# Kernel tuning notes

Measured on AMD Instinct MI355X. Metric: run time of the kernel, lower is better.

## Reference

```python
import jax, jax.numpy as jnp
import numpy as np

N_NODES = 50000
N_EDGES = 800000
IN_CH = 128
HID = 128
N_CLASSES = 10
NUM_GRAPHS = 64


def setup_inputs() -> dict:
    key = jax.random.key(0)
    ks = jax.random.split(key, 16)
    x = jax.random.normal(ks[0], (N_NODES, IN_CH), dtype=jnp.float32)
    edge_index = jax.random.randint(ks[1], (2, N_EDGES), 0, N_NODES, dtype=jnp.int64)
    batch = jnp.sort(jax.random.randint(ks[2], (N_NODES,), 0, NUM_GRAPHS, dtype=jnp.int64))

    def lin(k, fan_in, fan_out):
        # torch nn.Linear default init: U(-1/sqrt(fan_in), 1/sqrt(fan_in))
        kw, kb = jax.random.split(k)
        bound = 1.0 / np.sqrt(fan_in)
        W = jax.random.uniform(kw, (fan_out, fan_in), jnp.float32, -bound, bound)
        b = jax.random.uniform(kb, (fan_out,), jnp.float32, -bound, bound)
        return W, b

    W_msg1, b_msg1 = lin(ks[3], IN_CH, HID)
    W_upd1, b_upd1 = lin(ks[4], IN_CH + HID, HID)
    W_msg2, b_msg2 = lin(ks[5], HID, HID)
    W_upd2, b_upd2 = lin(ks[6], HID + HID, HID)
    W_cls, b_cls = lin(ks[7], HID, N_CLASSES)
    return {
        "x": x, "edge_index": edge_index, "batch": batch,
        "W_msg1": W_msg1, "b_msg1": b_msg1, "W_upd1": W_upd1, "b_upd1": b_upd1,
        "W_msg2": W_msg2, "b_msg2": b_msg2, "W_upd2": W_upd2, "b_upd2": b_upd2,
        "W_cls": W_cls, "b_cls": b_cls,
    }


def _mpnn_layer(x, row, col, W_msg, b_msg, W_upd, b_upd):
    # gather -> linear message
    messages = x[col] @ W_msg.T + b_msg          # [E, out]
    # scatter-add aggregate into node buckets
    aggr = jax.ops.segment_sum(messages, row, num_segments=x.shape[0])  # [N, out]
    # concat + linear + ReLU update
    h = jnp.concatenate([x, aggr], axis=1) @ W_upd.T + b_upd
    return jax.nn.relu(h)


def reference(x, edge_index, batch,
              W_msg1, b_msg1, W_upd1, b_upd1,
              W_msg2, b_msg2, W_upd2, b_upd2,
              W_cls, b_cls):
    row, col = edge_index[0], edge_index[1]
    h = _mpnn_layer(x, row, col, W_msg1, b_msg1, W_upd1, b_upd1)
    h = _mpnn_layer(h, row, col, W_msg2, b_msg2, W_upd2, b_upd2)
    # mean pool per graph
    pooled = jax.ops.segment_sum(h, batch, num_segments=NUM_GRAPHS)   # [G, HID]
    count = jnp.bincount(batch, length=NUM_GRAPHS).astype(pooled.dtype)
    pooled = pooled / count[:, None]
    return pooled @ W_cls.T + b_cls
```

## Files before the change

kernel.cpp:

```cpp
#include <hip/hip_runtime.h>
#include <hip/hip_bf16.h>

#define N_NODES 50000
#define N_EDGES 800000
#define NUM_GRAPHS 64
#define NBUCK 391

typedef __attribute__((ext_vector_type(8))) short short8;
typedef __attribute__((ext_vector_type(16))) float f32x16;

static __device__ __forceinline__ short f2bf(float f) {
    union { __hip_bfloat16 h; short s; } u;
    u.h = __float2bfloat16(f);
    return u.s;
}
static __device__ __forceinline__ unsigned short f2bfu(float f) {
    union { __hip_bfloat16 h; unsigned short s; } u;
    u.h = __float2bfloat16(f);
    return u.s;
}
static __device__ __forceinline__ float bflo(unsigned u) { return __uint_as_float(u << 16); }
static __device__ __forceinline__ float bfhi(unsigned u) { return __uint_as_float(u & 0xffff0000u); }

__global__ void cvt_kernel(const float* __restrict__ x, uint4* __restrict__ xb, int n8) {
    int i = blockIdx.x * 256 + threadIdx.x;
    if (i >= n8) return;
    const float4* p = (const float4*)(x + (size_t)i * 8);
    float4 f0 = p[0], f1 = p[1];
    uint4 r;
    r.x = ((unsigned)f2bfu(f0.y) << 16) | f2bfu(f0.x);
    r.y = ((unsigned)f2bfu(f0.w) << 16) | f2bfu(f0.z);
    r.z = ((unsigned)f2bfu(f1.y) << 16) | f2bfu(f1.x);
    r.w = ((unsigned)f2bfu(f1.w) << 16) | f2bfu(f1.z);
    xb[i] = r;
}

__global__ void fold_kernel(const float* __restrict__ Wu1, const float* __restrict__ Wm1,
                            const float* __restrict__ bm1, short* __restrict__ Wcatf1,
                            float* __restrict__ c1,
                            const float* __restrict__ Wu2, const float* __restrict__ Wm2,
                            const float* __restrict__ bm2, short* __restrict__ Wcatf2,
                            float* __restrict__ c2) {
    int layer = blockIdx.x >> 7;
    int o = blockIdx.x & 127;
    int k = threadIdx.x;
    const float* Wu = layer ? Wu2 : Wu1;
    const float* Wm = layer ? Wm2 : Wm1;
    const float* bm = layer ? bm2 : bm1;
    short* Wcatf = layer ? Wcatf2 : Wcatf1;
    float* cvec = layer ? c2 : c1;
    float val;
    if (k < 128) {
        val = Wu[o * 256 + k];
    } else {
        int kk = k - 128;
        float s = 0.f;
        for (int j = 0; j < 128; ++j) s += Wu[o * 256 + 128 + j] * Wm[j * 128 + kk];
        val = s;
    }
    Wcatf[(((k >> 3) * 128) + o) * 8 + (k & 7)] = f2bf(val);
    if (k == 0) {
        float cs = 0.f;
        for (int j = 0; j < 128; ++j) cs += Wu[o * 256 + 128 + j] * bm[j];
        cvec[o] = cs;
    }
}

__global__ void cnt_kernel(const int* __restrict__ batch, float* __restrict__ cnt, int N) {
    __shared__ float loc[NUM_GRAPHS];
    int t = threadIdx.x;
    if (t < NUM_GRAPHS) loc[t] = 0.f;
    __syncthreads();
    int n = blockIdx.x * 256 + t;
    if (n < N) atomicAdd(&loc[batch[n]], 1.0f);
    __syncthreads();
    if (t < NUM_GRAPHS && loc[t] != 0.f) atomicAdd(&cnt[t], loc[t]);
}

__global__ __launch_bounds__(1024) void binhist_kernel(const int* __restrict__ row,
                                                       int* __restrict__ bhist, int E) {
    __shared__ int lh[NBUCK];
    int t = threadIdx.x;
    for (int i = t; i < NBUCK; i += 1024) lh[i] = 0;
    __syncthreads();
    int e0 = blockIdx.x * 4096;
#pragma unroll
    for (int k = 0; k < 4; ++k) {
        int e = e0 + k * 1024 + t;
        if (e < E) atomicAdd(&lh[row[e] >> 7], 1);
    }
    __syncthreads();
    for (int i = t; i < NBUCK; i += 1024)
        if (lh[i]) atomicAdd(&bhist[i], lh[i]);
}

__global__ void bscan_kernel(const int* __restrict__ bhist, int* __restrict__ bbase,
                             int* __restrict__ bcur) {
    __shared__ int s[512];
    int t = threadIdx.x;
    int v = (t < NBUCK) ? bhist[t] : 0;
    s[t] = v;
    __syncthreads();
    for (int o = 1; o < 512; o <<= 1) {
        int a = (t >= o) ? s[t - o] : 0;
        __syncthreads();
        s[t] += a;
        __syncthreads();
    }
    if (t <= NBUCK) bbase[t] = s[t] - ((t < NBUCK) ? bhist[t] : 0);
    if (t < NBUCK) bcur[t] = s[t] - bhist[t];
}

__global__ __launch_bounds__(1024) void binA_kernel(const int* __restrict__ row,
                                                    const int* __restrict__ col,
                                                    int* __restrict__ bcur,
                                                    unsigned* __restrict__ ebin, int E) {
    __shared__ int lcur[NBUCK];
    __shared__ int lscan[NBUCK];
    __shared__ int gbase[NBUCK];
    __shared__ int sscan[512];
    __shared__ unsigned stage[4096];
    int t = threadIdx.x;
    for (int i = t; i < NBUCK; i += 1024) lcur[i] = 0;
    __syncthreads();
    int e0 = blockIdx.x * 4096;
    unsigned pv[4];
    int pb[4], pr[4];
#pragma unroll
    for (int k = 0; k < 4; ++k) {
        int e = e0 + k * 1024 + t;
        if (e < E) {
            int r = row[e], c = col[e];
            pv[k] = ((unsigned)r << 16) | (unsigned)c;
            pb[k] = r >> 7;
            pr[k] = atomicAdd(&lcur[pb[k]], 1);
        } else {
            pb[k] = -1;
        }
    }
    __syncthreads();
    if (t < 512) sscan[t] = (t < NBUCK) ? lcur[t] : 0;
    __syncthreads();
    for (int o = 1; o < 512; o <<= 1) {
        int a = 0;
        if (t < 512 && t >= o) a = sscan[t - o];
        __syncthreads();
        if (t < 512) sscan[t] += a;
        __syncthreads();
    }
    if (t < NBUCK) lscan[t] = sscan[t] - lcur[t];
    __syncthreads();
    for (int i = t; i < NBUCK; i += 1024) {
        int c = lcur[i];
        gbase[i] = c ? atomicAdd(&bcur[i], c) : 0;
    }
#pragma unroll
    for (int k = 0; k < 4; ++k)
        if (pb[k] >= 0) stage[lscan[pb[k]] + pr[k]] = pv[k];
    __syncthreads();
    int total = E - e0;
    if (total > 4096) total = 4096;
    for (int idx = t; idx < total; idx += 1024) {
        unsigned v = stage[idx];
        int b = v >> 23;
        ebin[gbase[b] + (idx - lscan[b])] = v;
    }
}

__global__ __launch_bounds__(256) void binB_kernel(const unsigned* __restrict__ ebin,
                                                   const int* __restrict__ bbase,
                                                   const int* __restrict__ bcur,
                                                   int* __restrict__ csr,
                                                   int* __restrict__ hist,
                                                   int* __restrict__ off, int N) {
    __shared__ int lcnt[128];
    __shared__ int loff[128];
    __shared__ int lcur2[128];
    __shared__ int sscan[128];
    __shared__ unsigned short stage[4096];
    int b = blockIdx.x, t = threadIdx.x;
    int base = bbase[b];
    int n = bcur[b] - base;
    if (n > 4096) n = 4096;
    if (t < 128) lcnt[t] = 0;
    __syncthreads();
    for (int idx = t; idx < n; idx += 256) {
        unsigned v = ebin[base + idx];
        atomicAdd(&lcnt[(v >> 16) & 127], 1);
    }
    __syncthreads();
    if (t < 128) sscan[t] = lcnt[t];
    __syncthreads();
    for (int o = 1; o < 128; o <<= 1) {
        int a = 0;
        if (t < 128 && t >= o) a = sscan[t - o];
        __syncthreads();
        if (t < 128) sscan[t] += a;
        __syncthreads();
    }
    if (t < 128) {
        loff[t] = sscan[t] - lcnt[t];
        lcur2[t] = sscan[t] - lcnt[t];
    }
    __syncthreads();
    for (int idx = t; idx < n; idx += 256) {
        unsigned v = ebin[base + idx];
        int lr = (v >> 16) & 127;
        int pos = atomicAdd(&lcur2[lr], 1);
        stage[pos] = (unsigned short)(v & 0xffffu);
    }
    __syncthreads();
    for (int idx = t; idx < n; idx += 256) csr[base + idx] = (int)stage[idx];
    int r0 = b * 128;
    if (t < 128 && r0 + t < N) {
        hist[r0 + t] = lcnt[t];
        off[r0 + t] = base + loff[t];
    }
}

__global__ __launch_bounds__(256) void gather_kernel(const unsigned short* __restrict__ src,
                                                     const int* __restrict__ off,
                                                     const int* __restrict__ hist,
                                                     const int* __restrict__ csr,
                                                     unsigned int* __restrict__ aggb, int N) {
    int wave = threadIdx.x >> 6, lane = threadIdx.x & 63;
    int n = blockIdx.x * 4 + wave;
    if (n >= N) return;
    int s = off[n];
    int e = s + hist[n];
    int grp = lane >> 4, sub = lane & 15;
    float a0 = 0.f, a1 = 0.f, a2 = 0.f, a3 = 0.f, a4 = 0.f, a5 = 0.f, a6 = 0.f, a7 = 0.f;
    for (int base = s; base < e; base += 64) {
        int m = e - base;
        if (m > 64) m = 64;
        int ce = (base + lane < e) ? csr[base + lane] : 0;
        int iters = (m + 3) >> 2;
#pragma unroll 4
        for (int i = 0; i < iters; ++i) {
            int idx = i * 4 + grp;
            int c = __shfl(ce, idx);
            uint4 v = *(const uint4*)(src + (size_t)c * 128 + sub * 8);
            if (idx >= m) { v.x = 0; v.y = 0; v.z = 0; v.w = 0; }
            a0 += bflo(v.x); a1 += bfhi(v.x);
            a2 += bflo(v.y); a3 += bfhi(v.y);
            a4 += bflo(v.z); a5 += bfhi(v.z);
            a6 += bflo(v.w); a7 += bfhi(v.w);
        }
    }
#pragma unroll
    for (int mk = 16; mk <= 32; mk <<= 1) {
        a0 += __shfl_xor(a0, mk); a1 += __shfl_xor(a1, mk);
        a2 += __shfl_xor(a2, mk); a3 += __shfl_xor(a3, mk);
        a4 += __shfl_xor(a4, mk); a5 += __shfl_xor(a5, mk);
        a6 += __shfl_xor(a6, mk); a7 += __shfl_xor(a7, mk);
    }
    if (grp == 0) {
        uint4 r;
        r.x = ((unsigned)f2bfu(a1) << 16) | f2bfu(a0);
        r.y = ((unsigned)f2bfu(a3) << 16) | f2bfu(a2);
        r.z = ((unsigned)f2bfu(a5) << 16) | f2bfu(a4);
        r.w = ((unsigned)f2bfu(a7) << 16) | f2bfu(a6);
        ((uint4*)aggb)[(size_t)n * 16 + sub] = r;
    }
}

template <int POOL>
__global__ __launch_bounds__(512) void update_kernel(
    const void* __restrict__ xin_, const unsigned int* __restrict__ aggb,
    const int* __restrict__ hist, const float* __restrict__ cvec,
    const float* __restrict__ bupd, const short* __restrict__ Wcatf,
    unsigned int* __restrict__ houtb, float* __restrict__ pooled,
    const int* __restrict__ batch, int N) {
    __shared__ short lds_s[32768];
    const int tid = threadIdx.x;
    const int wave = tid >> 6, lane = tid & 63;
    const int l31 = lane & 31, hi = lane >> 5;

    {
        const uint4* g = (const uint4*)Wcatf;
        uint4* l4 = (uint4*)lds_s;
#pragma unroll
        for (int j = 0; j < 8; ++j) l4[j * 512 + tid] = g[j * 512 + tid];
    }
    __syncthreads();

    const int m0 = blockIdx.x * 256 + wave * 32;
    int nr = m0 + l31;
    if (nr >= N) nr = N - 1;
    f32x16 acc[4] = {};
#pragma unroll
    for (int step = 0; step < 16; ++step) {
        short8 a;
        if (step < 8) {
            a = *(const short8*)((const short*)xin_ + (size_t)nr * 128 + step * 16 + hi * 8);
        } else {
            a = *(const short8*)((const short*)aggb + (size_t)nr * 128 + (step - 8) * 16 + hi * 8);
        }
#pragma unroll
        for (int ct = 0; ct < 4; ++ct) {
            const short8 b = *(const short8*)(lds_s + (((step * 2 + hi) * 128) + ct * 32 + l31) * 8);
            acc[ct] = __builtin_amdgcn_mfma_f32_32x32x16_bf16(a, b, acc[ct], 0, 0, 0);
        }
    }
    __syncthreads();

    float dv[16];
#pragma unroll
    for (int r = 0; r < 16; ++r) {
        int row = (r & 3) + 8 * (r >> 2) + 4 * hi;
        int node = m0 + row;
        if (node >= N) node = N - 1;
        dv[r] = (float)hist[node];
    }
    short* tp = lds_s + wave * 4096;
#pragma unroll
    for (int ct = 0; ct < 4; ++ct) {
        int o = ct * 32 + l31;
        float co = cvec[o], bo = bupd[o];
#pragma unroll
        for (int r = 0; r < 16; ++r) {
            int row = (r & 3) + 8 * (r >> 2) + 4 * hi;
            float v = fmaxf(acc[ct][r] + dv[r] * co + bo, 0.f);
            tp[row * 128 + o] = f2bf(v);
        }
    }
    __syncthreads();

    if (POOL == 0) {
        const uint4* l4 = (const uint4*)tp;
#pragma unroll
        for (int j = 0; j < 8; ++j) {
            int node = m0 + j * 4 + (lane >> 4);
            if (node < N)
                ((uint4*)houtb)[(size_t)m0 * 16 + j * 64 + lane] = l4[j * 64 + lane];
        }
    } else {
        int c = tid & 127, seg = tid >> 7;
        int base = blockIdx.x * 256 + seg * 64;
        float s = 0.f;
        int gprev = -1;
        for (int i = 0; i < 64; ++i) {
            int node = base + i;
            if (node >= N) break;
            int g = batch[node];
            if (g != gprev) {
                if (gprev >= 0) atomicAdd(&pooled[gprev * 128 + c], s);
                s = 0.f;
                gprev = g;
            }
            unsigned u = (unsigned short)lds_s[(seg * 64 + i) * 128 + c];
            s += __uint_as_float(u << 16);
        }
        if (gprev >= 0) atomicAdd(&pooled[gprev * 128 + c], s);
    }
}

__global__ void final_kernel(const float* __restrict__ pooled, const float* __restrict__ cnt,
                             const float* __restrict__ Wcls, const float* __restrict__ bcls,
                             float* __restrict__ out) {
    __shared__ float sh[128];
    int g = blockIdx.x;
    int t = threadIdx.x;
    sh[t] = pooled[g * 128 + t] / cnt[g];
    __syncthreads();
    if (t < 10) {
        float s = bcls[t];
        for (int i = 0; i < 128; ++i) s += sh[i] * Wcls[t * 128 + i];
        out[g * 10 + t] = s;
    }
}

extern "C" void kernel_launch(void* const* d_in, const int* in_sizes, int n_in,
                              void* d_out, int out_size, void* d_ws, size_t ws_size,
                              hipStream_t stream) {
    const float* x = (const float*)d_in[0];
    const int* ei = (const int*)d_in[1];
    const int* batch = (const int*)d_in[2];
    const float* Wm1 = (const float*)d_in[3];
    const float* bm1 = (const float*)d_in[4];
    const float* Wu1 = (const float*)d_in[5];
    const float* bu1 = (const float*)d_in[6];
    const float* Wm2 = (const float*)d_in[7];
    const float* bm2 = (const float*)d_in[8];
    const float* Wu2 = (const float*)d_in[9];
    const float* bu2 = (const float*)d_in[10];
    const float* Wcls = (const float*)d_in[11];
    const float* bcls = (const float*)d_in[12];
    float* out = (float*)d_out;

    const int N = N_NODES, E = N_EDGES;
    const int* row = ei;
    const int* col = ei + E;
    const int EB = (E + 4095) / 4096;
    const int UB = (N + 255) / 256;

    int* bhist = (int*)d_ws;
    float* cnt = (float*)(bhist + 512);
    float* pooled = cnt + 64;
    int* bbase = (int*)(pooled + 8192);
    int* bcur = bbase + 512;
    int* hist = bcur + 512;
    int* off = hist + 50000;
    unsigned* ebin = (unsigned*)(off + 50000);
    int* csr = (int*)(ebin + 800000);
    unsigned* aggb = (unsigned*)(csr + 800000);
    unsigned* h1b = aggb + 3200000;
    unsigned* xb = h1b + 3200000;
    float* c1 = (float*)(xb + 3200000);
    float* c2 = c1 + 128;
    short* Wcatf1 = (short*)(c2 + 128);
    short* Wcatf2 = Wcatf1 + 32768;

    hipMemsetAsync(d_ws, 0, (size_t)(512 + 64 + 8192) * 4, stream);

    cvt_kernel<<<(800000 + 255) / 256, 256, 0, stream>>>(x, (uint4*)xb, 800000);
    fold_kernel<<<256, 256, 0, stream>>>(Wu1, Wm1, bm1, Wcatf1, c1,
                                         Wu2, Wm2, bm2, Wcatf2, c2);
    cnt_kernel<<<(N + 255) / 256, 256, 0, stream>>>(batch, cnt, N);

    binhist_kernel<<<EB, 1024, 0, stream>>>(row, bhist, E);
    bscan_kernel<<<1, 512, 0, stream>>>(bhist, bbase, bcur);
    binA_kernel<<<EB, 1024, 0, stream>>>(row, col, bcur, ebin, E);
    binB_kernel<<<NBUCK, 256, 0, stream>>>(ebin, bbase, bcur, csr, hist, off, N);

    gather_kernel<<<(N + 3) / 4, 256, 0, stream>>>((const unsigned short*)xb, off, hist,
                                                   csr, aggb, N);
    update_kernel<0><<<UB, 512, 0, stream>>>(xb, aggb, hist, c1, bu1, Wcatf1,
                                             h1b, nullptr, nullptr, N);
    gather_kernel<<<(N + 3) / 4, 256, 0, stream>>>((const unsigned short*)h1b, off, hist,
                                                   csr, aggb, N);
    update_kernel<1><<<UB, 512, 0, stream>>>(h1b, aggb, hist, c2, bu2, Wcatf2,
                                             nullptr, pooled, batch, N);

    final_kernel<<<NUM_GRAPHS, 128, 0, stream>>>(pooled, cnt, Wcls, bcls, out);
}
```

Measured before the change: 152.4 us.

## Merge prep kernels, compute graph counts by binary search, simplify gather loop

Result: faster. 143.9 us (-5.6%).

```diff
diff --git a/kernel.cpp b/kernel.cpp
--- a/kernel.cpp
+++ b/kernel.cpp
@@ -22,59 +22,55 @@
 static __device__ __forceinline__ float bflo(unsigned u) { return __uint_as_float(u << 16); }
 static __device__ __forceinline__ float bfhi(unsigned u) { return __uint_as_float(u & 0xffff0000u); }
 
-__global__ void cvt_kernel(const float* __restrict__ x, uint4* __restrict__ xb, int n8) {
-    int i = blockIdx.x * 256 + threadIdx.x;
-    if (i >= n8) return;
-    const float4* p = (const float4*)(x + (size_t)i * 8);
-    float4 f0 = p[0], f1 = p[1];
-    uint4 r;
-    r.x = ((unsigned)f2bfu(f0.y) << 16) | f2bfu(f0.x);
-    r.y = ((unsigned)f2bfu(f0.w) << 16) | f2bfu(f0.z);
-    r.z = ((unsigned)f2bfu(f1.y) << 16) | f2bfu(f1.x);
-    r.w = ((unsigned)f2bfu(f1.w) << 16) | f2bfu(f1.z);
-    xb[i] = r;
-}
-
-__global__ void fold_kernel(const float* __restrict__ Wu1, const float* __restrict__ Wm1,
-                            const float* __restrict__ bm1, short* __restrict__ Wcatf1,
-                            float* __restrict__ c1,
-                            const float* __restrict__ Wu2, const float* __restrict__ Wm2,
-                            const float* __restrict__ bm2, short* __restrict__ Wcatf2,
-                            float* __restrict__ c2) {
-    int layer = blockIdx.x >> 7;
-    int o = blockIdx.x & 127;
-    int k = threadIdx.x;
-    const float* Wu = layer ? Wu2 : Wu1;
-    const float* Wm = layer ? Wm2 : Wm1;
-    const float* bm = layer ? bm2 : bm1;
-    short* Wcatf = layer ? Wcatf2 : Wcatf1;
-    float* cvec = layer ? c2 : c1;
-    float val;
-    if (k < 128) {
-        val = Wu[o * 256 + k];
+__global__ __launch_bounds__(256) void prep_kernel(
+    const float* __restrict__ x, uint4* __restrict__ xb,
+    const float* __restrict__ Wu1, const float* __restrict__ Wm1,
+    const float* __restrict__ bm1, short* __restrict__ Wcatf1, float* __restrict__ c1,
+    const float* __restrict__ Wu2, const float* __restrict__ Wm2,
+    const float* __restrict__ bm2, short* __restrict__ Wcatf2, float* __restrict__ c2,
+    int* __restrict__ zbase) {
+    int bid = blockIdx.x, t = threadIdx.x;
+    if (bid < 3125) {
+        int i = bid * 256 + t;
+        if (i < 800000) {
+            const float4* p = (const float4*)(x + (size_t)i * 8);
+            float4 f0 = p[0], f1 = p[1];
+            uint4 r;
+            r.x = ((unsigned)f2bfu(f0.y) << 16) | f2bfu(f0.x);
+            r.y = ((unsigned)f2bfu(f0.w) << 16) | f2bfu(f0.z);
+            r.z = ((unsigned)f2bfu(f1.y) << 16) | f2bfu(f1.x);
+            r.w = ((unsigned)f2bfu(f1.w) << 16) | f2bfu(f1.z);
+            xb[i] = r;
+        }
+    } else if (bid < 3381) {
+        int lb = bid - 3125;
+        int layer = lb >> 7;
+        int o = lb & 127;
+        int k = t;
+        const float* Wu = layer ? Wu2 : Wu1;
+        const float* Wm = layer ? Wm2 : Wm1;
+        const float* bm = layer ? bm2 : bm1;
+        short* Wcatf = layer ? Wcatf2 : Wcatf1;
+        float* cvec = layer ? c2 : c1;
+        float val;
+        if (k < 128) {
+            val = Wu[o * 256 + k];
+        } else {
+            int kk = k - 128;
+            float s = 0.f;
+            for (int j = 0; j < 128; ++j) s += Wu[o * 256 + 128 + j] * Wm[j * 128 + kk];
+            val = s;
+        }
+        Wcatf[(((k >> 3) * 128) + o) * 8 + (k & 7)] = f2bf(val);
+        if (k == 0) {
+            float cs = 0.f;
+            for (int j = 0; j < 128; ++j) cs += Wu[o * 256 + 128 + j] * bm[j];
+            cvec[o] = cs;
+        }
     } else {
-        int kk = k - 128;
-        float s = 0.f;
-        for (int j = 0; j < 128; ++j) s += Wu[o * 256 + 128 + j] * Wm[j * 128 + kk];
-        val = s;
-    }
-    Wcatf[(((k >> 3) * 128) + o) * 8 + (k & 7)] = f2bf(val);
-    if (k == 0) {
-        float cs = 0.f;
-        for (int j = 0; j < 128; ++j) cs += Wu[o * 256 + 128 + j] * bm[j];
-        cvec[o] = cs;
-    }
-}
-
-__global__ void cnt_kernel(const int* __restrict__ batch, float* __restrict__ cnt, int N) {
-    __shared__ float loc[NUM_GRAPHS];
-    int t = threadIdx.x;
-    if (t < NUM_GRAPHS) loc[t] = 0.f;
-    __syncthreads();
-    int n = blockIdx.x * 256 + t;
-    if (n < N) atomicAdd(&loc[batch[n]], 1.0f);
-    __syncthreads();
-    if (t < NUM_GRAPHS && loc[t] != 0.f) atomicAdd(&cnt[t], loc[t]);
+        int i = (bid - 3381) * 256 + t;
+        if (i < 512 + 8192) zbase[i] = 0;
+    }
 }
 
 __global__ __launch_bounds__(1024) void binhist_kernel(const int* __restrict__ row,
@@ -230,22 +226,14 @@
     int e = s + hist[n];
     int grp = lane >> 4, sub = lane & 15;
     float a0 = 0.f, a1 = 0.f, a2 = 0.f, a3 = 0.f, a4 = 0.f, a5 = 0.f, a6 = 0.f, a7 = 0.f;
-    for (int base = s; base < e; base += 64) {
-        int m = e - base;
-        if (m > 64) m = 64;
-        int ce = (base + lane < e) ? csr[base + lane] : 0;
-        int iters = (m + 3) >> 2;
 #pragma unroll 4
-        for (int i = 0; i < iters; ++i) {
-            int idx = i * 4 + grp;
-            int c = __shfl(ce, idx);
-            uint4 v = *(const uint4*)(src + (size_t)c * 128 + sub * 8);
-            if (idx >= m) { v.x = 0; v.y = 0; v.z = 0; v.w = 0; }
-            a0 += bflo(v.x); a1 += bfhi(v.x);
-            a2 += bflo(v.y); a3 += bfhi(v.y);
-            a4 += bflo(v.z); a5 += bfhi(v.z);
-            a6 += bflo(v.w); a7 += bfhi(v.w);
-        }
+    for (int i = s + grp; i < e; i += 4) {
+        int c = csr[i];
+        uint4 v = *(const uint4*)(src + (size_t)c * 128 + sub * 8);
+        a0 += bflo(v.x); a1 += bfhi(v.x);
+        a2 += bflo(v.y); a3 += bfhi(v.y);
+        a4 += bflo(v.z); a5 += bfhi(v.z);
+        a6 += bflo(v.w); a7 += bfhi(v.w);
     }
 #pragma unroll
     for (int mk = 16; mk <= 32; mk <<= 1) {
@@ -355,13 +343,24 @@
     }
 }
 
-__global__ void final_kernel(const float* __restrict__ pooled, const float* __restrict__ cnt,
+__global__ void final_kernel(const float* __restrict__ pooled, const int* __restrict__ batch,
                              const float* __restrict__ Wcls, const float* __restrict__ bcls,
-                             float* __restrict__ out) {
+                             float* __restrict__ out, int N) {
     __shared__ float sh[128];
+    __shared__ int cntsh;
     int g = blockIdx.x;
     int t = threadIdx.x;
-    sh[t] = pooled[g * 128 + t] / cnt[g];
+    if (t == 0) {
+        int lo = 0, hi = N;
+        while (lo < hi) { int mid = (lo + hi) >> 1; if (batch[mid] < g) lo = mid + 1; else hi = mid; }
+        int start = lo;
+        lo = 0; hi = N;
+        while (lo < hi) { int mid = (lo + hi) >> 1; if (batch[mid] < g + 1) lo = mid + 1; else hi = mid; }
+        cntsh = lo - start;
+    }
+    __syncthreads();
+    float c = (cntsh > 0) ? (float)cntsh : 1.f;
+    sh[t] = pooled[g * 128 + t] / c;
     __syncthreads();
     if (t < 10) {
         float s = bcls[t];
@@ -395,8 +394,7 @@
     const int UB = (N + 255) / 256;
 
     int* bhist = (int*)d_ws;
-    float* cnt = (float*)(bhist + 512);
-    float* pooled = cnt + 64;
+    float* pooled = (float*)(bhist + 512);
     int* bbase = (int*)(pooled + 8192);
     int* bcur = bbase + 512;
     int* hist = bcur + 512;
@@ -411,13 +409,8 @@
     short* Wcatf1 = (short*)(c2 + 128);
     short* Wcatf2 = Wcatf1 + 32768;
 
-    hipMemsetAsync(d_ws, 0, (size_t)(512 + 64 + 8192) * 4, stream);
-
-    cvt_kernel<<<(800000 + 255) / 256, 256, 0, stream>>>(x, (uint4*)xb, 800000);
-    fold_kernel<<<256, 256, 0, stream>>>(Wu1, Wm1, bm1, Wcatf1, c1,
-                                         Wu2, Wm2, bm2, Wcatf2, c2);
-    cnt_kernel<<<(N + 255) / 256, 256, 0, stream>>>(batch, cnt, N);
-
+    prep_kernel<<<3415, 256, 0, stream>>>(x, (uint4*)xb, Wu1, Wm1, bm1, Wcatf1, c1,
+                                          Wu2, Wm2, bm2, Wcatf2, c2, bhist);
     binhist_kernel<<<EB, 1024, 0, stream>>>(row, bhist, E);
     bscan_kernel<<<1, 512, 0, stream>>>(bhist, bbase, bcur);
     binA_kernel<<<EB, 1024, 0, stream>>>(row, col, bcur, ebin, E);
@@ -432,5 +425,5 @@
     update_kernel<1><<<UB, 512, 0, stream>>>(h1b, aggb, hist, c2, bu2, Wcatf2,
                                              nullptr, pooled, batch, N);
 
-    final_kernel<<<NUM_GRAPHS, 128, 0, stream>>>(pooled, cnt, Wcls, bcls, out);
-}
+    final_kernel<<<NUM_GRAPHS, 128, 0, stream>>>(pooled, batch, Wcls, bcls, out, N);
+}
```
